# Kernel optimization log

Hardware: AMD Instinct MI355X
Metric: run time of the kernel (lower is better)

The kernel has to match this reference:

```python
import jax, jax.numpy as jnp
import numpy as np

N_NODES = 50000
IN_CH, HID_CH, OUT_CH = 128, 128, 64
N_EDGES = 800000


def setup_inputs() -> dict:
    key = jax.random.key(0)
    k = jax.random.split(key, 6)
    x = jax.random.normal(k[0], (N_NODES, IN_CH), dtype=jnp.float32)
    edge_index = jax.random.randint(k[1], (2, N_EDGES), 0, N_NODES, dtype=jnp.int64)
    # Glorot-ish init for weights
    W1 = jax.random.normal(k[2], (IN_CH, HID_CH), dtype=jnp.float32) * (1.0 / np.sqrt(IN_CH))
    b1 = jnp.zeros((HID_CH,), dtype=jnp.float32)
    W2 = jax.random.normal(k[3], (HID_CH, OUT_CH), dtype=jnp.float32) * (1.0 / np.sqrt(HID_CH))
    b2 = jnp.zeros((OUT_CH,), dtype=jnp.float32)
    return {"x": x, "edge_index": edge_index, "W1": W1, "b1": b1, "W2": W2, "b2": b2}


def _gcn_conv(x, src, dst, W, b, n_nodes):
    """PyG GCNConv: linear, add self-loops, symmetric deg^-1/2 normalization, scatter-add."""
    h = x @ W  # [N, F_out]
    loop = jnp.arange(n_nodes, dtype=src.dtype)
    s = jnp.concatenate([src, loop])  # [E+N]
    d = jnp.concatenate([dst, loop])
    # in-degree on target nodes (including self-loops), edge weight = 1
    deg = jnp.zeros((n_nodes,), dtype=h.dtype).at[d].add(1.0)
    dinv = jnp.where(deg > 0, jax.lax.rsqrt(deg), 0.0)
    norm = dinv[s] * dinv[d]  # [E+N]
    msg = h[s] * norm[:, None]  # [E+N, F_out]
    out = jax.ops.segment_sum(msg, d, num_segments=n_nodes)
    return out + b


def reference(x, edge_index, W1, b1, W2, b2):
    src, dst = edge_index[0], edge_index[1]
    h = _gcn_conv(x, src, dst, W1, b1, N_NODES)
    h = jax.nn.relu(h)
    # dropout in eval mode -> identity
    out = _gcn_conv(h, src, dst, W2, b2, N_NODES)
    return out
```

## Files before the change

### kernel.cpp

```cpp
#include <hip/hip_runtime.h>

typedef __attribute__((ext_vector_type(8))) short bf16x8;
typedef __attribute__((ext_vector_type(4))) float f32x4;

constexpr int NN = 50000;
constexpr int NE = 800000;
constexpr int C1 = 128;
constexpr int C2 = 64;
constexpr int NBK = 196;
constexpr int EPB = 2048;
constexpr int NBLK = (NE + EPB - 1) / EPB;
constexpr int MT = NN / 16;
constexpr int CAP = 8192;
constexpr int GB = (NN + 3) / 4;

constexpr int K1G = 1024;
constexpr int MM1_NW = (K1G - NBLK) * 4;
constexpr int K3G = 1792;

__device__ __forceinline__ unsigned short f2bf(float f) {
    unsigned int u = __float_as_uint(f);
    u += 0x7FFFu + ((u >> 16) & 1u);
    return (unsigned short)(u >> 16);
}
__device__ __forceinline__ float2 bf2f(unsigned int u) {
    return make_float2(__uint_as_float(u << 16), __uint_as_float(u & 0xFFFF0000u));
}
__device__ __forceinline__ unsigned int pk2(float a, float b) {
    return (unsigned int)f2bf(a) | ((unsigned int)f2bf(b) << 16);
}
__device__ __forceinline__ bf16x8 pack8(float4 a, float4 b) {
    bf16x8 r;
    r[0] = (short)f2bf(a.x); r[1] = (short)f2bf(a.y);
    r[2] = (short)f2bf(a.z); r[3] = (short)f2bf(a.w);
    r[4] = (short)f2bf(b.x); r[5] = (short)f2bf(b.y);
    r[6] = (short)f2bf(b.z); r[7] = (short)f2bf(b.w);
    return r;
}

struct BinSmem {
    int lhist[NBK];
    int ls[256];
    int lcur[NBK];
    unsigned int lbuf[EPB];
};

__device__ void bin_work(const int* __restrict__ src, const int* __restrict__ dst,
                         unsigned int* __restrict__ ebuf, int* __restrict__ localOff,
                         BinSmem& S) {
    const int t = threadIdx.x;
    const int base = blockIdx.x * EPB;
    if (t < NBK) S.lhist[t] = 0;
    __syncthreads();
    int b[8]; unsigned int p[8];
    #pragma unroll
    for (int i = 0; i < 8; i++) {
        int e = base + i * 256 + t;
        if (e < NE) {
            int s = src[e], d = dst[e];
            b[i] = d >> 8;
            p[i] = ((unsigned int)(d & 255) << 16) | (unsigned int)s;
            atomicAdd(&S.lhist[b[i]], 1);
        } else b[i] = -1;
    }
    __syncthreads();
    int v = (t < NBK) ? S.lhist[t] : 0;
    S.ls[t] = v;
    __syncthreads();
    #pragma unroll
    for (int d = 1; d < 256; d <<= 1) {
        int u = (t >= d) ? S.ls[t - d] : 0;
        __syncthreads();
        S.ls[t] += u;
        __syncthreads();
    }
    if (t < NBK) {
        S.lcur[t] = S.ls[t] - v;
        localOff[blockIdx.x * 200 + t] = S.ls[t] - v;
    }
    if (t == NBK - 1) localOff[blockIdx.x * 200 + NBK] = S.ls[t];
    __syncthreads();
    #pragma unroll
    for (int i = 0; i < 8; i++) {
        if (b[i] >= 0) {
            int lp = atomicAdd(&S.lcur[b[i]], 1);
            S.lbuf[lp] = p[i];
        }
    }
    __syncthreads();
    #pragma unroll
    for (int i = 0; i < 8; i++)
        ebuf[base + i * 256 + t] = S.lbuf[i * 256 + t];
}

__device__ void mm1_work(const float* __restrict__ x, const float* __restrict__ W,
                         unsigned short* __restrict__ g1,
                         unsigned short (&wl)[4][8][64][8]) {
    const int t = threadIdx.x;
    for (int i = 0; i < 64; i++) {
        int idx = i * 256 + t;
        int k = idx >> 7, n = idx & 127;
        wl[k >> 5][n >> 4][((k >> 3) & 3) * 16 + (n & 15)][k & 7] = f2bf(W[idx]);
    }
    __syncthreads();
    const int lane = t & 63, lm = lane & 15, quad = lane >> 4;

    bf16x8 bfr[4][8];
    #pragma unroll
    for (int s = 0; s < 4; s++)
        #pragma unroll
        for (int nt = 0; nt < 8; nt++)
            bfr[s][nt] = *(const bf16x8*)&wl[s][nt][lane][0];

    const int widx = (blockIdx.x - NBLK) * 4 + (t >> 6);
    for (int tile = widx; tile < MT; tile += MM1_NW) {
        int row0 = tile << 4;
        const float* xr = x + (size_t)(row0 + lm) * 128 + quad * 8;
        bf16x8 af[4];
        #pragma unroll
        for (int s = 0; s < 4; s++) {
            float4 p = *(const float4*)(xr + s * 32);
            float4 q = *(const float4*)(xr + s * 32 + 4);
            af[s] = pack8(p, q);
        }
        f32x4 acc[8];
        #pragma unroll
        for (int nt = 0; nt < 8; nt++) acc[nt] = (f32x4){0.f, 0.f, 0.f, 0.f};
        #pragma unroll
        for (int s = 0; s < 4; s++)
            #pragma unroll
            for (int nt = 0; nt < 8; nt++)
                acc[nt] = __builtin_amdgcn_mfma_f32_16x16x32_bf16(af[s], bfr[s][nt],
                                                                  acc[nt], 0, 0, 0);
        #pragma unroll
        for (int nt = 0; nt < 8; nt++)
            #pragma unroll
            for (int r = 0; r < 4; r++)
                g1[(size_t)(row0 + quad * 4 + r) * 128 + nt * 16 + lm] = f2bf(acc[nt][r]);
    }
}

__global__ __launch_bounds__(256, 2) void k1_kernel(const int* __restrict__ src,
                                                    const int* __restrict__ dst,
                                                    unsigned int* __restrict__ ebuf,
                                                    int* __restrict__ localOff,
                                                    const float* __restrict__ x,
                                                    const float* __restrict__ W1,
                                                    unsigned short* __restrict__ g1) {
    __shared__ union { BinSmem b; unsigned short wl[4][8][64][8]; } sm;
    if (blockIdx.x < NBLK) bin_work(src, dst, ebuf, localOff, sm.b);
    else                   mm1_work(x, W1, g1, sm.wl);
}

__global__ __launch_bounds__(256) void place_kernel(const unsigned int* __restrict__ ebuf,
                                                    const int* __restrict__ localOff,
                                                    unsigned short* __restrict__ esrc,
                                                    int* __restrict__ cnt,
                                                    int* __restrict__ off,
                                                    float* __restrict__ dinv,
                                                    unsigned short* __restrict__ g1) {
    __shared__ unsigned int lbuf[CAP];
    __shared__ int lhist[256];
    __shared__ int ls[256];
    __shared__ int lcur[256];
    __shared__ int red[256];
    const int t = threadIdx.x;
    const int bkt = blockIdx.x;
    const int node0 = bkt << 8;
    const int nnodes = min(256, NN - node0);

    const int j0 = 2 * t, j1 = 2 * t + 1;
    int s0 = 0, l0 = 0, s1 = 0, l1 = 0;
    if (j0 < NBLK) { s0 = localOff[j0 * 200 + bkt]; l0 = localOff[j0 * 200 + bkt + 1] - s0; }
    if (j1 < NBLK) { s1 = localOff[j1 * 200 + bkt]; l1 = localOff[j1 * 200 + bkt + 1] - s1; }

    red[t] = s0 + s1;
    ls[t] = l0 + l1;
    lhist[t] = 0;
    __syncthreads();
    #pragma unroll
    for (int d = 1; d < 256; d <<= 1) {
        int u = (t >= d) ? ls[t - d] : 0;
        int r = (t + d < 256) ? red[t + d] : 0;
        __syncthreads();
        ls[t] += u;
        red[t] += r;
        __syncthreads();
    }
    const int segBase = red[0];
    const int total = ls[255];
    const int base0 = ls[t] - (l0 + l1);
    const int base1 = base0 + l0;
    const bool fits = (total <= CAP);

    if (fits) {
        const unsigned int* q0 = ebuf + j0 * EPB + s0;
        for (int k = 0; k < l0; k++) lbuf[base0 + k] = q0[k];
        const unsigned int* q1 = ebuf + j1 * EPB + s1;
        for (int k = 0; k < l1; k++) lbuf[base1 + k] = q1[k];
        __syncthreads();
        for (int k = t; k < total; k += 256) atomicAdd(&lhist[lbuf[k] >> 16], 1);
    } else {
        const unsigned int* q0 = ebuf + j0 * EPB + s0;
        for (int k = 0; k < l0; k++) atomicAdd(&lhist[q0[k] >> 16], 1);
        const unsigned int* q1 = ebuf + j1 * EPB + s1;
        for (int k = 0; k < l1; k++) atomicAdd(&lhist[q1[k] >> 16], 1);
    }
    __syncthreads();
    int v = lhist[t];
    ls[t] = v;
    __syncthreads();
    #pragma unroll
    for (int d = 1; d < 256; d <<= 1) {
        int u = (t >= d) ? ls[t - d] : 0;
        __syncthreads();
        ls[t] += u;
        __syncthreads();
    }
    int ex = ls[t] - v;
    lcur[t] = ex;
    if (t < nnodes) {
        cnt[node0 + t] = v;
        off[node0 + t] = segBase + ex;
        dinv[node0 + t] = rsqrtf((float)v + 1.0f);
    }
    __syncthreads();
    if (fits) {
        for (int k = t; k < total; k += 256) {
            unsigned int pp = lbuf[k];
            int lp = atomicAdd(&lcur[pp >> 16], 1);
            esrc[segBase + lp] = (unsigned short)(pp & 0xFFFFu);
        }
    } else {
        const unsigned int* q0 = ebuf + j0 * EPB + s0;
        for (int k = 0; k < l0; k++) {
            unsigned int pp = q0[k];
            int lp = atomicAdd(&lcur[pp >> 16], 1);
            esrc[segBase + lp] = (unsigned short)(pp & 0xFFFFu);
        }
        const unsigned int* q1 = ebuf + j1 * EPB + s1;
        for (int k = 0; k < l1; k++) {
            unsigned int pp = q1[k];
            int lp = atomicAdd(&lcur[pp >> 16], 1);
            esrc[segBase + lp] = (unsigned short)(pp & 0xFFFFu);
        }
    }
    const int w = t >> 6, lane = t & 63;
    unsigned int* g1u = (unsigned int*)g1;
    for (int r = w; r < nnodes; r += 4) {
        const float dn = dinv[node0 + r];
        const size_t a = (size_t)(node0 + r) * 64 + lane;
        float2 p = bf2f(g1u[a]);
        g1u[a] = pk2(dn * p.x, dn * p.y);
    }
}

__global__ __launch_bounds__(256) void gmm_kernel(const unsigned short* __restrict__ g1,
                                                  const unsigned short* __restrict__ esrc,
                                                  const int* __restrict__ off,
                                                  const int* __restrict__ cnt,
                                                  const float* __restrict__ dinv,
                                                  const float* __restrict__ b1,
                                                  const float* __restrict__ W2,
                                                  unsigned short* __restrict__ g2) {
    __shared__ unsigned short wl2[4][4][64][8];
    __shared__ unsigned short x2t[16][136];
    const int t = threadIdx.x;
    for (int i = 0; i < 32; i++) {
        int idx = i * 256 + t;
        int k = idx >> 6, n = idx & 63;
        wl2[k >> 5][n >> 4][((k >> 3) & 3) * 16 + (n & 15)][k & 7] = f2bf(W2[idx]);
    }
    const int lane = t & 63, w = t >> 6, lm = lane & 15, quad = lane >> 4;
    const unsigned int* G = (const unsigned int*)g1;
    const float2 bb = ((const float2*)b1)[lane];

    for (int tile = blockIdx.x; tile < MT; tile += K3G) {
        __syncthreads();
        #pragma unroll 1
        for (int k4 = 0; k4 < 4; k4++) {
            const int n = tile * 16 + w * 4 + k4;
            float2 ps = bf2f(G[(size_t)n * 64 + lane]);
            float a0 = ps.x, a1 = ps.y;
            float c0 = 0.f, c1 = 0.f;
            const int s0 = off[n], c = cnt[n];
            for (int base = 0; base < c; base += 64) {
                const int m = min(64, c - base);
                int vidx = 0;
                if (lane < m) vidx = esrc[s0 + base + lane];
                int i = 0;
                for (; i + 3 < m; i += 4) {
                    int sA = __shfl(vidx, i),     sB = __shfl(vidx, i + 1);
                    int sC = __shfl(vidx, i + 2), sD = __shfl(vidx, i + 3);
                    unsigned int vA = G[(size_t)sA * 64 + lane];
                    unsigned int vB = G[(size_t)sB * 64 + lane];
                    unsigned int vC = G[(size_t)sC * 64 + lane];
                    unsigned int vD = G[(size_t)sD * 64 + lane];
                    float2 pA = bf2f(vA); a0 += pA.x; a1 += pA.y;
                    float2 pB = bf2f(vB); c0 += pB.x; c1 += pB.y;
                    float2 pC = bf2f(vC); a0 += pC.x; a1 += pC.y;
                    float2 pD = bf2f(vD); c0 += pD.x; c1 += pD.y;
                }
                for (; i < m; i++) {
                    int sA = __shfl(vidx, i);
                    float2 pA = bf2f(G[(size_t)sA * 64 + lane]);
                    a0 += pA.x; a1 += pA.y;
                }
            }
            a0 += c0; a1 += c1;
            const float sc = dinv[n];
            const float o0 = fmaxf(sc * a0 + bb.x, 0.f);
            const float o1 = fmaxf(sc * a1 + bb.y, 0.f);
            ((unsigned int*)&x2t[w * 4 + k4][0])[lane] = pk2(o0, o1);
        }
        __syncthreads();
        const int row0 = tile << 4;
        bf16x8 af[4];
        #pragma unroll
        for (int s = 0; s < 4; s++)
            af[s] = *(const bf16x8*)&x2t[lm][quad * 8 + s * 32];
        f32x4 acc = (f32x4){0.f, 0.f, 0.f, 0.f};
        #pragma unroll
        for (int s = 0; s < 4; s++) {
            bf16x8 bfr = *(const bf16x8*)&wl2[s][w][lane][0];
            acc = __builtin_amdgcn_mfma_f32_16x16x32_bf16(af[s], bfr, acc, 0, 0, 0);
        }
        float4 dv = *(const float4*)(dinv + row0 + quad * 4);
        float dvv[4] = {dv.x, dv.y, dv.z, dv.w};
        #pragma unroll
        for (int r = 0; r < 4; r++)
            g2[(size_t)(row0 + quad * 4 + r) * 64 + w * 16 + lm] = f2bf(acc[r] * dvv[r]);
    }
}

__global__ __launch_bounds__(256) void gather2_kernel(const unsigned short* __restrict__ g2,
                                                      const unsigned short* __restrict__ esrc,
                                                      const int* __restrict__ off,
                                                      const int* __restrict__ cnt,
                                                      const float* __restrict__ dinv,
                                                      const float* __restrict__ b2,
                                                      float* __restrict__ out) {
    const int n = blockIdx.x * 4 + (threadIdx.x >> 6);
    if (n >= NN) return;
    const int lane = threadIdx.x & 63;
    const unsigned short* G = g2;
    float a0 = __uint_as_float((unsigned int)G[(size_t)n * 64 + lane] << 16);
    float c0 = 0.f;
    const int s0 = off[n], c = cnt[n];
    for (int base = 0; base < c; base += 64) {
        const int m = min(64, c - base);
        int vidx = 0;
        if (lane < m) vidx = esrc[s0 + base + lane];
        int i = 0;
        for (; i + 3 < m; i += 4) {
            int sA = __shfl(vidx, i),     sB = __shfl(vidx, i + 1);
            int sC = __shfl(vidx, i + 2), sD = __shfl(vidx, i + 3);
            unsigned short vA = G[(size_t)sA * 64 + lane];
            unsigned short vB = G[(size_t)sB * 64 + lane];
            unsigned short vC = G[(size_t)sC * 64 + lane];
            unsigned short vD = G[(size_t)sD * 64 + lane];
            a0 += __uint_as_float((unsigned int)vA << 16);
            c0 += __uint_as_float((unsigned int)vB << 16);
            a0 += __uint_as_float((unsigned int)vC << 16);
            c0 += __uint_as_float((unsigned int)vD << 16);
        }
        for (; i < m; i++) {
            int sA = __shfl(vidx, i);
            a0 += __uint_as_float((unsigned int)G[(size_t)sA * 64 + lane] << 16);
        }
    }
    a0 += c0;
    out[(size_t)n * 64 + lane] = dinv[n] * a0 + b2[lane];
}

extern "C" void kernel_launch(void* const* d_in, const int* in_sizes, int n_in,
                              void* d_out, int out_size, void* d_ws, size_t ws_size,
                              hipStream_t stream) {
    const float* x  = (const float*)d_in[0];
    const int* edges = (const int*)d_in[1];
    const float* W1 = (const float*)d_in[2];
    const float* b1 = (const float*)d_in[3];
    const float* W2 = (const float*)d_in[4];
    const float* b2 = (const float*)d_in[5];
    const int* src = edges;
    const int* dst = edges + NE;

    int* localOff  = (int*)d_ws;
    unsigned int* ebuf = (unsigned int*)(localOff + 78208);
    unsigned short* esrc = (unsigned short*)(ebuf + (size_t)NBLK * EPB);
    int* cnt       = (int*)(esrc + 800768);
    int* off       = cnt + 50048;
    float* dinv    = (float*)(off + 50048);
    unsigned short* g1 = (unsigned short*)(dinv + 50048);
    unsigned short* g2 = g1 + (size_t)NN * C1;
    float* out = (float*)d_out;

    k1_kernel<<<K1G, 256, 0, stream>>>(src, dst, ebuf, localOff, x, W1, g1);
    place_kernel<<<NBK, 256, 0, stream>>>(ebuf, localOff, esrc, cnt, off, dinv, g1);
    gmm_kernel<<<K3G, 256, 0, stream>>>(g1, esrc, off, cnt, dinv, b1, W2, g2);
    gather2_kernel<<<GB, 256, 0, stream>>>(g2, esrc, off, cnt, dinv, b2, out);
}
```

Baseline: 188.4 us.

## Split fused gather+GEMM into separate gather1 and mm2 kernels, fold dinv into gather

The fused layer-1 aggregation + layer-2 GEMM kernel is split into a per-node gather kernel (one wave per node, full grid) and a separate MFMA GEMM kernel that keeps all W2 fragments in registers and computes all 64 output columns per wave. The source-side dinv scaling of g1, which used to be an in-place pass in place_kernel, is now applied inside the gather through a per-edge dinv lookup broadcast with shuffles. This targets the load imbalance and low occupancy of the fused tile loop and removes a read-modify-write pass over g1. In exchange it adds an extra kernel launch and an N×128 bf16 intermediate written and re-read through global memory.

```diff
diff --git a/kernel.cpp b/kernel.cpp
--- a/kernel.cpp
+++ b/kernel.cpp
@@ -13,10 +13,11 @@
 constexpr int MT = NN / 16;
 constexpr int CAP = 8192;
 constexpr int GB = (NN + 3) / 4;
+constexpr int MMB = 500;
+constexpr int MMWAVES = MMB * 4;
 
 constexpr int K1G = 1024;
 constexpr int MM1_NW = (K1G - NBLK) * 4;
-constexpr int K3G = 1792;
 
 __device__ __forceinline__ unsigned short f2bf(float f) {
     unsigned int u = __float_as_uint(f);
@@ -157,8 +158,7 @@
                                                     unsigned short* __restrict__ esrc,
                                                     int* __restrict__ cnt,
                                                     int* __restrict__ off,
-                                                    float* __restrict__ dinv,
-                                                    unsigned short* __restrict__ g1) {
+                                                    float* __restrict__ dinv) {
     __shared__ unsigned int lbuf[CAP];
     __shared__ int lhist[256];
     __shared__ int ls[256];
@@ -245,91 +245,105 @@
             esrc[segBase + lp] = (unsigned short)(pp & 0xFFFFu);
         }
     }
-    const int w = t >> 6, lane = t & 63;
-    unsigned int* g1u = (unsigned int*)g1;
-    for (int r = w; r < nnodes; r += 4) {
-        const float dn = dinv[node0 + r];
-        const size_t a = (size_t)(node0 + r) * 64 + lane;
-        float2 p = bf2f(g1u[a]);
-        g1u[a] = pk2(dn * p.x, dn * p.y);
-    }
-}
-
-__global__ __launch_bounds__(256) void gmm_kernel(const unsigned short* __restrict__ g1,
-                                                  const unsigned short* __restrict__ esrc,
-                                                  const int* __restrict__ off,
-                                                  const int* __restrict__ cnt,
-                                                  const float* __restrict__ dinv,
-                                                  const float* __restrict__ b1,
-                                                  const float* __restrict__ W2,
-                                                  unsigned short* __restrict__ g2) {
-    __shared__ unsigned short wl2[4][4][64][8];
-    __shared__ unsigned short x2t[16][136];
+}
+
+__global__ __launch_bounds__(256) void gather1_kernel(const unsigned short* __restrict__ g1,
+                                                      const unsigned short* __restrict__ esrc,
+                                                      const int* __restrict__ off,
+                                                      const int* __restrict__ cnt,
+                                                      const float* __restrict__ dinv,
+                                                      const float* __restrict__ b1,
+                                                      unsigned short* __restrict__ x2) {
+    const int n = blockIdx.x * 4 + (threadIdx.x >> 6);
+    if (n >= NN) return;
+    const int lane = threadIdx.x & 63;
+    const unsigned int* G = (const unsigned int*)g1;
+    const float dn = dinv[n];
+    float2 ps = bf2f(G[(size_t)n * 64 + lane]);
+    float a0 = dn * ps.x, a1 = dn * ps.y;
+    float c0 = 0.f, c1 = 0.f;
+    const int s0 = off[n], c = cnt[n];
+    for (int base = 0; base < c; base += 64) {
+        const int m = min(64, c - base);
+        int vidx = 0; float vdin = 0.f;
+        if (lane < m) {
+            vidx = esrc[s0 + base + lane];
+            vdin = dinv[vidx];
+        }
+        int i = 0;
+        for (; i + 3 < m; i += 4) {
+            int sA = __shfl(vidx, i),     sB = __shfl(vidx, i + 1);
+            int sC = __shfl(vidx, i + 2), sD = __shfl(vidx, i + 3);
+            float dA = __shfl(vdin, i),     dB = __shfl(vdin, i + 1);
+            float dC = __shfl(vdin, i + 2), dD = __shfl(vdin, i + 3);
+            unsigned int vA = G[(size_t)sA * 64 + lane];
+            unsigned int vB = G[(size_t)sB * 64 + lane];
+            unsigned int vC = G[(size_t)sC * 64 + lane];
+            unsigned int vD = G[(size_t)sD * 64 + lane];
+            float2 pA = bf2f(vA); a0 = fmaf(dA, pA.x, a0); a1 = fmaf(dA, pA.y, a1);
+            float2 pB = bf2f(vB); c0 = fmaf(dB, pB.x, c0); c1 = fmaf(dB, pB.y, c1);
+            float2 pC = bf2f(vC); a0 = fmaf(dC, pC.x, a0); a1 = fmaf(dC, pC.y, a1);
+            float2 pD = bf2f(vD); c0 = fmaf(dD, pD.x, c0); c1 = fmaf(dD, pD.y, c1);
+        }
+        for (; i < m; i++) {
+            int sA = __shfl(vidx, i);
+            float dA = __shfl(vdin, i);
+            float2 pA = bf2f(G[(size_t)sA * 64 + lane]);
+            a0 = fmaf(dA, pA.x, a0); a1 = fmaf(dA, pA.y, a1);
+        }
+    }
+    a0 += c0; a1 += c1;
+    const float2 bb = ((const float2*)b1)[lane];
+    const float o0 = fmaxf(dn * a0 + bb.x, 0.f);
+    const float o1 = fmaxf(dn * a1 + bb.y, 0.f);
+    ((unsigned int*)x2)[(size_t)n * 64 + lane] = pk2(o0, o1);
+}
+
+__global__ __launch_bounds__(256, 2) void mm2_kernel(const unsigned short* __restrict__ x2,
+                                                     const float* __restrict__ W,
+                                                     const float* __restrict__ dinv,
+                                                     unsigned short* __restrict__ g2) {
+    __shared__ unsigned short wl[4][4][64][8];
     const int t = threadIdx.x;
     for (int i = 0; i < 32; i++) {
         int idx = i * 256 + t;
         int k = idx >> 6, n = idx & 63;
-        wl2[k >> 5][n >> 4][((k >> 3) & 3) * 16 + (n & 15)][k & 7] = f2bf(W2[idx]);
-    }
-    const int lane = t & 63, w = t >> 6, lm = lane & 15, quad = lane >> 4;
-    const unsigned int* G = (const unsigned int*)g1;
-    const float2 bb = ((const float2*)b1)[lane];
-
-    for (int tile = blockIdx.x; tile < MT; tile += K3G) {
-        __syncthreads();
-        #pragma unroll 1
-        for (int k4 = 0; k4 < 4; k4++) {
-            const int n = tile * 16 + w * 4 + k4;
-            float2 ps = bf2f(G[(size_t)n * 64 + lane]);
-            float a0 = ps.x, a1 = ps.y;
-            float c0 = 0.f, c1 = 0.f;
-            const int s0 = off[n], c = cnt[n];
-            for (int base = 0; base < c; base += 64) {
-                const int m = min(64, c - base);
-                int vidx = 0;
-                if (lane < m) vidx = esrc[s0 + base + lane];
-                int i = 0;
-                for (; i + 3 < m; i += 4) {
-                    int sA = __shfl(vidx, i),     sB = __shfl(vidx, i + 1);
-                    int sC = __shfl(vidx, i + 2), sD = __shfl(vidx, i + 3);
-                    unsigned int vA = G[(size_t)sA * 64 + lane];
-                    unsigned int vB = G[(size_t)sB * 64 + lane];
-                    unsigned int vC = G[(size_t)sC * 64 + lane];
-                    unsigned int vD = G[(size_t)sD * 64 + lane];
-                    float2 pA = bf2f(vA); a0 += pA.x; a1 += pA.y;
-                    float2 pB = bf2f(vB); c0 += pB.x; c1 += pB.y;
-                    float2 pC = bf2f(vC); a0 += pC.x; a1 += pC.y;
-                    float2 pD = bf2f(vD); c0 += pD.x; c1 += pD.y;
-                }
-                for (; i < m; i++) {
-                    int sA = __shfl(vidx, i);
-                    float2 pA = bf2f(G[(size_t)sA * 64 + lane]);
-                    a0 += pA.x; a1 += pA.y;
-                }
-            }
-            a0 += c0; a1 += c1;
-            const float sc = dinv[n];
-            const float o0 = fmaxf(sc * a0 + bb.x, 0.f);
-            const float o1 = fmaxf(sc * a1 + bb.y, 0.f);
-            ((unsigned int*)&x2t[w * 4 + k4][0])[lane] = pk2(o0, o1);
-        }
-        __syncthreads();
-        const int row0 = tile << 4;
+        wl[k >> 5][n >> 4][((k >> 3) & 3) * 16 + (n & 15)][k & 7] = f2bf(W[idx]);
+    }
+    __syncthreads();
+    const int lane = t & 63, lm = lane & 15, quad = lane >> 4;
+
+    bf16x8 bfr[4][4];
+    #pragma unroll
+    for (int s = 0; s < 4; s++)
+        #pragma unroll
+        for (int nt = 0; nt < 4; nt++)
+            bfr[s][nt] = *(const bf16x8*)&wl[s][nt][lane][0];
+
+    int wg = blockIdx.x * 4 + (t >> 6);
+    for (int tile = wg; tile < MT; tile += MMWAVES) {
+        int row0 = tile << 4;
+        const bf16x8* xr = (const bf16x8*)(x2 + (size_t)(row0 + lm) * 128 + quad * 8);
         bf16x8 af[4];
         #pragma unroll
+        for (int s = 0; s < 4; s++) af[s] = xr[s * 4];
+        f32x4 acc[4];
+        #pragma unroll
+        for (int nt = 0; nt < 4; nt++) acc[nt] = (f32x4){0.f, 0.f, 0.f, 0.f};
+        #pragma unroll
         for (int s = 0; s < 4; s++)
-            af[s] = *(const bf16x8*)&x2t[lm][quad * 8 + s * 32];
-        f32x4 acc = (f32x4){0.f, 0.f, 0.f, 0.f};
-        #pragma unroll
-        for (int s = 0; s < 4; s++) {
-            bf16x8 bfr = *(const bf16x8*)&wl2[s][w][lane][0];
-            acc = __builtin_amdgcn_mfma_f32_16x16x32_bf16(af[s], bfr, acc, 0, 0, 0);
-        }
+            #pragma unroll
+            for (int nt = 0; nt < 4; nt++)
+                acc[nt] = __builtin_amdgcn_mfma_f32_16x16x32_bf16(af[s], bfr[s][nt],
+                                                                  acc[nt], 0, 0, 0);
         float4 dv = *(const float4*)(dinv + row0 + quad * 4);
         float dvv[4] = {dv.x, dv.y, dv.z, dv.w};
         #pragma unroll
-        for (int r = 0; r < 4; r++)
-            g2[(size_t)(row0 + quad * 4 + r) * 64 + w * 16 + lm] = f2bf(acc[r] * dvv[r]);
+        for (int nt = 0; nt < 4; nt++)
+            #pragma unroll
+            for (int r = 0; r < 4; r++)
+                g2[(size_t)(row0 + quad * 4 + r) * 64 + nt * 16 + lm] =
+                    f2bf(acc[nt][r] * dvv[r]);
     }
 }
 
@@ -392,11 +406,13 @@
     int* off       = cnt + 50048;
     float* dinv    = (float*)(off + 50048);
     unsigned short* g1 = (unsigned short*)(dinv + 50048);
-    unsigned short* g2 = g1 + (size_t)NN * C1;
+    unsigned short* x2 = g1 + (size_t)NN * C1;
+    unsigned short* g2 = g1;
     float* out = (float*)d_out;
 
     k1_kernel<<<K1G, 256, 0, stream>>>(src, dst, ebuf, localOff, x, W1, g1);
-    place_kernel<<<NBK, 256, 0, stream>>>(ebuf, localOff, esrc, cnt, off, dinv, g1);
-    gmm_kernel<<<K3G, 256, 0, stream>>>(g1, esrc, off, cnt, dinv, b1, W2, g2);
+    place_kernel<<<NBK, 256, 0, stream>>>(ebuf, localOff, esrc, cnt, off, dinv);
+    gather1_kernel<<<GB, 256, 0, stream>>>(g1, esrc, off, cnt, dinv, b1, x2);
+    mm2_kernel<<<MMB, 256, 0, stream>>>(x2, W2, dinv, g2);
     gather2_kernel<<<GB, 256, 0, stream>>>(g2, esrc, off, cnt, dinv, b2, out);
 }
```

New measurement: 179.6 us, median of 2. 1.05x faster.
